# Optimization experiments

Hardware: AMD Instinct MI355X
Metric: run time of the kernel (lower is better)

## Reference

```python
import jax, jax.numpy as jnp
import numpy as np

N_NODES = 50000
N_EDGES = 600000
DIM_H = 128
LN_EPS = 1e-5


def setup_inputs() -> dict:
    key = jax.random.key(0)
    ks = jax.random.split(key, 8)
    s = 1.0 / np.sqrt(DIM_H)
    return {
        "nodes": jax.random.normal(ks[0], (N_NODES, DIM_H), jnp.float32),
        "W_msg": jax.random.normal(ks[1], (DIM_H, DIM_H), jnp.float32) * s,
        "b_msg": jnp.zeros((DIM_H,), jnp.float32),
        "w_ih": jax.random.normal(ks[2], (3 * DIM_H, DIM_H), jnp.float32) * s,
        "w_hh": jax.random.normal(ks[3], (3 * DIM_H, DIM_H), jnp.float32) * s,
        "b_ih": jnp.zeros((3 * DIM_H,), jnp.float32),
        "b_hh": jnp.zeros((3 * DIM_H,), jnp.float32),
        "ln_gamma": jnp.ones((DIM_H,), jnp.float32),
        "ln_beta": jnp.zeros((DIM_H,), jnp.float32),
        "edge_src": jax.random.randint(ks[4], (N_EDGES,), 0, N_NODES, jnp.int32),
        "edge_dst": jax.random.randint(ks[5], (N_EDGES,), 0, N_NODES, jnp.int32),
    }


def _layer_norm(x, gamma, beta):
    mu = jnp.mean(x, axis=-1, keepdims=True)
    var = jnp.mean(jnp.square(x - mu), axis=-1, keepdims=True)
    return gamma * (x - mu) * jax.lax.rsqrt(var + LN_EPS) + beta


def reference(nodes, W_msg, b_msg, w_ih, w_hh, b_ih, b_hh, ln_gamma, ln_beta,
              edge_src, edge_dst):
    n_nodes = nodes.shape[0]
    # send_and_recv: per-edge message from source node, sum-reduce at dest
    msg_e = nodes[edge_src] @ W_msg.T + b_msg            # [E, H] (irregular gather)
    messages = jax.ops.segment_sum(msg_e, edge_dst, num_segments=n_nodes)  # [N, H]
    # global connection: add mean node feature
    msg = messages + jnp.mean(nodes, axis=0)
    # single-step GRU (torch gate layout: r, z, n)
    gi = msg @ w_ih.T + b_ih                             # [N, 3H]
    gh = nodes @ w_hh.T + b_hh                           # [N, 3H]
    i_r, i_z, i_n = jnp.split(gi, 3, axis=-1)
    h_r, h_z, h_n = jnp.split(gh, 3, axis=-1)
    r = jax.nn.sigmoid(i_r + h_r)
    z = jax.nn.sigmoid(i_z + h_z)
    n = jnp.tanh(i_n + r * h_n)
    h_next = (1.0 - z) * n + z * nodes
    # LayerNorm then post-GRU spatial residual with messages
    out = _layer_norm(h_next, ln_gamma, ln_beta)
    out = out + messages
    return out
```

## Files before the change

### kernel.cpp

```cpp
#include <hip/hip_runtime.h>
#include <hip/hip_bf16.h>

#define N_NODES 50000
#define N_EDGES 600000
#define DIM_H   128
#define NPAD    50048
#define NB_SCAN 196

typedef __attribute__((ext_vector_type(8))) short bf16x8;
typedef __attribute__((ext_vector_type(4))) float f32x4;
typedef __attribute__((ext_vector_type(4))) short short4v;

__device__ __forceinline__ short f2bs(float f) {
    __hip_bfloat16 h = __float2bfloat16(f);
    return *reinterpret_cast<short*>(&h);
}
__device__ __forceinline__ float bs2f(short s) {
    unsigned u = ((unsigned)(unsigned short)s) << 16;
    return __builtin_bit_cast(float, u);
}
__device__ __forceinline__ float sigm(float x) { return 1.f / (1.f + __expf(-x)); }
__device__ __forceinline__ float tanh_f(float x) {
    return 2.f / (1.f + __expf(-2.f * x)) - 1.f;
}
__device__ __forceinline__ unsigned pk2(float a, float b) {
    return ((unsigned)(unsigned short)f2bs(b) << 16) | (unsigned)(unsigned short)f2bs(a);
}
__device__ __forceinline__ float unlo(unsigned u) { return bs2f((short)(u & 0xffffu)); }
__device__ __forceinline__ float unhi(unsigned u) { return bs2f((short)(u >> 16)); }

__device__ __forceinline__ void dma16(const void* g, const void* lds_uniform) {
    __builtin_amdgcn_global_load_lds(
        (const __attribute__((address_space(1))) void*)g,
        (__attribute__((address_space(3))) void*)(unsigned)(unsigned long long)lds_uniform,
        16, 0, 0);
}

__global__ __launch_bounds__(256) void prep_k(const float* __restrict__ wmsg,
                                              const float* __restrict__ wih,
                                              const float* __restrict__ whh,
                                              short* __restrict__ wmsgB,
                                              short* __restrict__ wihB,
                                              short* __restrict__ whhB,
                                              int* __restrict__ cnt,
                                              float* __restrict__ colsum,
                                              short* __restrict__ aggTail,
                                              short* __restrict__ nodesTail) {
    int i = blockIdx.x * 256 + threadIdx.x;
    if (i < 16384) wmsgB[i] = f2bs(wmsg[i]);
    if (i < 49152) { wihB[i] = f2bs(wih[i]); whhB[i] = f2bs(whh[i]); }
    if (i < N_NODES) cnt[i] = 0;
    if (i < 128) colsum[i] = 0.f;
    if (i < 1536) {
        short4v z = {0, 0, 0, 0};
        *(short4v*)(aggTail   + i * 4) = z;
        *(short4v*)(nodesTail + i * 4) = z;
    }
}

__global__ __launch_bounds__(256) void colsum_k(const float* __restrict__ nodes,
                                                float* __restrict__ colsum,
                                                short* __restrict__ nodesB) {
    __shared__ float red[8][128];
    const int tid = threadIdx.x;
    const int cg = tid & 31;
    const int rl = tid >> 5;
    float4 acc = {0.f, 0.f, 0.f, 0.f};
    for (int r = blockIdx.x * 8 + rl; r < N_NODES; r += gridDim.x * 8) {
        float4 v = *(const float4*)(nodes + (size_t)r * DIM_H + cg * 4);
        acc.x += v.x; acc.y += v.y; acc.z += v.z; acc.w += v.w;
        *(short4v*)(nodesB + (size_t)r * DIM_H + cg * 4) =
            (short4v){f2bs(v.x), f2bs(v.y), f2bs(v.z), f2bs(v.w)};
    }
    *(float4*)&red[rl][cg * 4] = acc;
    __syncthreads();
    if (tid < 128) {
        float s = 0.f;
#pragma unroll
        for (int i = 0; i < 8; ++i) s += red[i][tid];
        unsafeAtomicAdd(&colsum[tid], s);
    }
}

__global__ __launch_bounds__(256) void hist_k(const int* __restrict__ edst,
                                              int* __restrict__ cnt) {
    int e = (blockIdx.x * 256 + threadIdx.x) * 4;
    if (e + 3 < N_EDGES) {
        int4 d = *(const int4*)(edst + e);
        atomicAdd(&cnt[d.x], 1); atomicAdd(&cnt[d.y], 1);
        atomicAdd(&cnt[d.z], 1); atomicAdd(&cnt[d.w], 1);
    } else {
        for (; e < N_EDGES; ++e) atomicAdd(&cnt[edst[e]], 1);
    }
}

__global__ __launch_bounds__(256) void bsum_k(const int* __restrict__ cnt,
                                              int* __restrict__ bsum) {
    const int t = threadIdx.x;
    int i = blockIdx.x * 256 + t;
    int v = (i < N_NODES) ? cnt[i] : 0;
#pragma unroll
    for (int o = 32; o; o >>= 1) v += __shfl_xor(v, o, 64);
    __shared__ int w4[4];
    if ((t & 63) == 0) w4[t >> 6] = v;
    __syncthreads();
    if (t == 0) bsum[blockIdx.x] = w4[0] + w4[1] + w4[2] + w4[3];
}

__global__ __launch_bounds__(256) void scan2_k(const int* __restrict__ cnt,
                                               const int* __restrict__ bsum,
                                               int* __restrict__ rowptr,
                                               int* __restrict__ pos) {
    const int b = blockIdx.x, t = threadIdx.x;
    const int lane = t & 63, w = t >> 6;
    __shared__ int red[4];
    __shared__ int wsum[4];

    int ov = (t < b) ? bsum[t] : 0;
#pragma unroll
    for (int o = 32; o; o >>= 1) ov += __shfl_xor(ov, o, 64);
    if (lane == 0) red[w] = ov;
    __syncthreads();
    const int offset = red[0] + red[1] + red[2] + red[3];

    int i = b * 256 + t;
    int v = (i < N_NODES) ? cnt[i] : 0;
    int x = v;
#pragma unroll
    for (int o = 1; o < 64; o <<= 1) {
        int y = __shfl_up(x, o, 64);
        if (lane >= o) x += y;
    }
    if (lane == 63) wsum[w] = x;
    __syncthreads();
    int woff = 0;
#pragma unroll
    for (int j = 0; j < 4; ++j)
        if (j < w) woff += wsum[j];
    int excl = offset + woff + (x - v);
    if (i < N_NODES) { rowptr[i] = excl; pos[i] = excl; }
    if (i == N_NODES - 1) rowptr[N_NODES] = excl + v;
}

__global__ __launch_bounds__(256) void reorder_k(const int* __restrict__ esrc,
                                                 const int* __restrict__ edst,
                                                 int* __restrict__ pos,
                                                 int* __restrict__ ssrc) {
    int e = (blockIdx.x * 256 + threadIdx.x) * 4;
    if (e + 3 < N_EDGES) {
        int4 s = *(const int4*)(esrc + e);
        int4 d = *(const int4*)(edst + e);
        ssrc[atomicAdd(&pos[d.x], 1)] = s.x;
        ssrc[atomicAdd(&pos[d.y], 1)] = s.y;
        ssrc[atomicAdd(&pos[d.z], 1)] = s.z;
        ssrc[atomicAdd(&pos[d.w], 1)] = s.w;
    } else {
        for (; e < N_EDGES; ++e) {
            int p = atomicAdd(&pos[edst[e]], 1);
            ssrc[p] = esrc[e];
        }
    }
}

__global__ __launch_bounds__(256) void aggregate_k(const short* __restrict__ nodesB,
                                                   const int* __restrict__ rowptr,
                                                   const int* __restrict__ ssrc,
                                                   short* __restrict__ aggB) {
    const int wid = threadIdx.x >> 6;
    const int lane = threadIdx.x & 63;
    const int g = lane >> 4, l = lane & 15;
    const int n = blockIdx.x * 4 + wid;
    if (n >= N_NODES) return;
    const int s0 = rowptr[n], s1 = rowptr[n + 1];

    float accf[8] = {0.f, 0.f, 0.f, 0.f, 0.f, 0.f, 0.f, 0.f};
    int e = s0 + g;
    for (; e + 4 < s1; e += 8) {
        int sa = ssrc[e], sb = ssrc[e + 4];
        bf16x8 va = *(const bf16x8*)(nodesB + (size_t)sa * DIM_H + l * 8);
        bf16x8 vb = *(const bf16x8*)(nodesB + (size_t)sb * DIM_H + l * 8);
#pragma unroll
        for (int k = 0; k < 8; ++k) accf[k] += bs2f(va[k]) + bs2f(vb[k]);
    }
    if (e < s1) {
        int sa = ssrc[e];
        bf16x8 va = *(const bf16x8*)(nodesB + (size_t)sa * DIM_H + l * 8);
#pragma unroll
        for (int k = 0; k < 8; ++k) accf[k] += bs2f(va[k]);
    }
#pragma unroll
    for (int k = 0; k < 8; ++k) {
        accf[k] += __shfl_xor(accf[k], 32, 64);
        accf[k] += __shfl_xor(accf[k], 16, 64);
    }
    if (g == 0) {
        uint4 ov;
        ov.x = pk2(accf[0], accf[1]);
        ov.y = pk2(accf[2], accf[3]);
        ov.z = pk2(accf[4], accf[5]);
        ov.w = pk2(accf[6], accf[7]);
        *(uint4*)(aggB + (size_t)n * DIM_H + l * 8) = ov;
    }
}

__global__ __launch_bounds__(512) void fused_k(const short* __restrict__ aggB,
                                               const short* __restrict__ nodesB,
                                               const short* __restrict__ wmsgB,
                                               const short* __restrict__ wihB,
                                               const short* __restrict__ whhB,
                                               const float* __restrict__ bmsg,
                                               const float* __restrict__ bih,
                                               const float* __restrict__ bhh,
                                               const int* __restrict__ deg,
                                               const float* __restrict__ colsum,
                                               const float* __restrict__ gamma,
                                               const float* __restrict__ beta,
                                               float* __restrict__ out) {
    __shared__ short Ms[128 * 128];
    __shared__ short Wb[2][64 * 128];
    __shared__ float biasL[1280];

    const int tid = threadIdx.x;
    const int lane = tid & 63, w = tid >> 6;
    const int m0 = blockIdx.x * 128;
    const int r16 = lane & 15, qh = lane >> 4;
    const int wm = w * 16;
    const float invN = 1.0f / N_NODES;

    if (tid < 384) {
        biasL[tid]       = bih[tid];
        biasL[384 + tid] = bhh[tid];
    }
    if (tid < 128) {
        biasL[768  + tid] = bmsg[tid];
        biasL[896  + tid] = colsum[tid] * invN;
        biasL[1024 + tid] = gamma[tid];
        biasL[1152 + tid] = beta[tid];
    }

    bf16x8 aggF[4], nodF[4], msgF[4];
    const size_t rowA = (size_t)(m0 + wm + r16) * 128;
#pragma unroll
    for (int kt = 0; kt < 4; ++kt) {
        aggF[kt] = *(const bf16x8*)(aggB   + rowA + ((kt << 2) + qh) * 8);
        nodF[kt] = *(const bf16x8*)(nodesB + rowA + ((kt << 2) + qh) * 8);
    }
    int4 dgi = *(const int4*)(deg + m0 + wm + qh * 4);

#define STAGE_W(SRC, ROW0, BUF) do {                                         \
    _Pragma("unroll") for (int it = 0; it < 2; ++it) {                       \
        int c = w * 2 + it;                                                  \
        int s = c * 64 + lane;                                               \
        int r = s >> 4, q = s & 15;                                          \
        int g = q ^ (r & 15);                                                \
        dma16((SRC) + (((size_t)((ROW0) + r)) << 7) + (g << 3),              \
              &Wb[BUF][0] + (size_t)c * 512);                                \
    } } while (0)

    STAGE_W(wmsgB, 0, 0);

    f32x4 acc[2][4];
    unsigned rp[2][4][2], inp[2][4][2], np_[2][4][2];

#define CHUNK(BUF, AF, H, RST) do {                                          \
    _Pragma("unroll") for (int kt = 0; kt < 4; ++kt) {                       \
        const int sq = (((kt << 2) + qh) ^ r16) << 3;                        \
        bf16x8 b0 = *(const bf16x8*)&Wb[BUF][(r16     ) * 128 + sq];         \
        bf16x8 b1 = *(const bf16x8*)&Wb[BUF][(r16 + 16) * 128 + sq];         \
        bf16x8 b2 = *(const bf16x8*)&Wb[BUF][(r16 + 32) * 128 + sq];         \
        bf16x8 b3 = *(const bf16x8*)&Wb[BUF][(r16 + 48) * 128 + sq];         \
        f32x4 z4 = {0.f, 0.f, 0.f, 0.f};                                     \
        acc[H][0] = __builtin_amdgcn_mfma_f32_16x16x32_bf16(                 \
            AF[kt], b0, ((RST) && kt == 0) ? z4 : acc[H][0], 0, 0, 0);       \
        acc[H][1] = __builtin_amdgcn_mfma_f32_16x16x32_bf16(                 \
            AF[kt], b1, ((RST) && kt == 0) ? z4 : acc[H][1], 0, 0, 0);       \
        acc[H][2] = __builtin_amdgcn_mfma_f32_16x16x32_bf16(                 \
            AF[kt], b2, ((RST) && kt == 0) ? z4 : acc[H][2], 0, 0, 0);       \
        acc[H][3] = __builtin_amdgcn_mfma_f32_16x16x32_bf16(                 \
            AF[kt], b3, ((RST) && kt == 0) ? z4 : acc[H][3], 0, 0, 0);       \
    } } while (0)

    __syncthreads(); STAGE_W(wmsgB,  64, 1); CHUNK(0, aggF, 0, 1);
    __syncthreads(); STAGE_W(wihB,    0, 0); CHUNK(1, aggF, 1, 1);

    {
        float dgf[4];
        dgf[0] = (m0 + wm + qh * 4 + 0 < N_NODES) ? (float)dgi.x : 0.f;
        dgf[1] = (m0 + wm + qh * 4 + 1 < N_NODES) ? (float)dgi.y : 0.f;
        dgf[2] = (m0 + wm + qh * 4 + 2 < N_NODES) ? (float)dgi.z : 0.f;
        dgf[3] = (m0 + wm + qh * 4 + 3 < N_NODES) ? (float)dgi.w : 0.f;
#pragma unroll
        for (int h = 0; h < 2; ++h)
#pragma unroll
            for (int j = 0; j < 4; ++j) {
                int c = h * 64 + j * 16 + r16;
                float bm = biasL[768 + c], cs = biasL[896 + c];
#pragma unroll
                for (int rr = 0; rr < 4; ++rr) {
                    int lr = wm + qh * 4 + rr;
                    float v = acc[h][j][rr] + dgf[rr] * bm + cs;
                    int slot = (c >> 3) ^ (lr & 15);
                    Ms[lr * 128 + slot * 8 + (c & 7)] = f2bs(v);
                }
            }
#pragma unroll
        for (int kt = 0; kt < 4; ++kt) {
            int kg = (kt << 2) + qh;
            msgF[kt] = *(const bf16x8*)&Ms[(wm + r16) * 128 + ((kg ^ r16) << 3)];
        }
    }

    __syncthreads(); STAGE_W(wihB,   64, 1); CHUNK(0, msgF, 0, 1);
    __syncthreads(); STAGE_W(whhB,    0, 0); CHUNK(1, msgF, 1, 1);
    __syncthreads(); STAGE_W(whhB,   64, 1); CHUNK(0, nodF, 0, 0);
    __syncthreads(); STAGE_W(wihB,  256, 0); CHUNK(1, nodF, 1, 0);
#pragma unroll
    for (int h = 0; h < 2; ++h)
#pragma unroll
        for (int j = 0; j < 4; ++j) {
            int c = h * 64 + j * 16 + r16;
            float b0 = biasL[c] + biasL[384 + c];
            rp[h][j][0] = pk2(sigm(acc[h][j][0] + b0), sigm(acc[h][j][1] + b0));
            rp[h][j][1] = pk2(sigm(acc[h][j][2] + b0), sigm(acc[h][j][3] + b0));
        }

    __syncthreads(); STAGE_W(wihB,  320, 1); CHUNK(0, msgF, 0, 1);
    __syncthreads(); STAGE_W(whhB,  256, 0); CHUNK(1, msgF, 1, 1);
#pragma unroll
    for (int h = 0; h < 2; ++h)
#pragma unroll
        for (int j = 0; j < 4; ++j) {
            int c = h * 64 + j * 16 + r16;
            float bi = biasL[256 + c];
            inp[h][j][0] = pk2(acc[h][j][0] + bi, acc[h][j][1] + bi);
            inp[h][j][1] = pk2(acc[h][j][2] + bi, acc[h][j][3] + bi);
        }

    __syncthreads(); STAGE_W(whhB,  320, 1); CHUNK(0, nodF, 0, 1);
    __syncthreads(); STAGE_W(wihB,  128, 0); CHUNK(1, nodF, 1, 1);
#pragma unroll
    for (int h = 0; h < 2; ++h)
#pragma unroll
        for (int j = 0; j < 4; ++j) {
            int c = h * 64 + j * 16 + r16;
            float bh = biasL[640 + c];
            float n0 = tanh_f(unlo(inp[h][j][0]) + unlo(rp[h][j][0]) * (acc[h][j][0] + bh));
            float n1 = tanh_f(unhi(inp[h][j][0]) + unhi(rp[h][j][0]) * (acc[h][j][1] + bh));
            float n2 = tanh_f(unlo(inp[h][j][1]) + unlo(rp[h][j][1]) * (acc[h][j][2] + bh));
            float n3 = tanh_f(unhi(inp[h][j][1]) + unhi(rp[h][j][1]) * (acc[h][j][3] + bh));
            np_[h][j][0] = pk2(n0, n1);
            np_[h][j][1] = pk2(n2, n3);
        }

    __syncthreads(); STAGE_W(wihB,  192, 1); CHUNK(0, msgF, 0, 1);
    __syncthreads(); STAGE_W(whhB,  128, 0); CHUNK(1, msgF, 1, 1);
    __syncthreads(); STAGE_W(whhB,  192, 1); CHUNK(0, nodF, 0, 0);
    __syncthreads();                         CHUNK(1, nodF, 1, 0);

#pragma unroll
    for (int h = 0; h < 2; ++h)
#pragma unroll
        for (int j = 0; j < 4; ++j) {
            int c = h * 64 + j * 16 + r16;
            float b1 = biasL[128 + c] + biasL[512 + c];
#pragma unroll
            for (int rr = 0; rr < 4; ++rr) {
                int lr = wm + qh * 4 + rr;
                float hv = bs2f(nodesB[(size_t)(m0 + lr) * 128 + c]);
                float z = sigm(acc[h][j][rr] + b1);
                float nv = (rr & 1) ? unhi(np_[h][j][rr >> 1]) : unlo(np_[h][j][rr >> 1]);
                acc[h][j][rr] = (1.f - z) * nv + z * hv;
            }
        }

#pragma unroll
    for (int rr = 0; rr < 4; ++rr) {
        float s = 0.f, q2 = 0.f;
#pragma unroll
        for (int h = 0; h < 2; ++h)
#pragma unroll
            for (int j = 0; j < 4; ++j) {
                float v = acc[h][j][rr];
                s += v; q2 += v * v;
            }
#pragma unroll
        for (int o = 1; o < 16; o <<= 1) {
            s  += __shfl_xor(s, o, 64);
            q2 += __shfl_xor(q2, o, 64);
        }
        int lr = wm + qh * 4 + rr;
        int gm = m0 + lr;
        float mu = s * (1.0f / DIM_H);
        float var = q2 * (1.0f / DIM_H) - mu * mu;
        float rstd = rsqrtf(var + 1e-5f);
        if (gm < N_NODES) {
#pragma unroll
            for (int h = 0; h < 2; ++h)
#pragma unroll
                for (int j = 0; j < 4; ++j) {
                    int c = h * 64 + j * 16 + r16;
                    int slot = (c >> 3) ^ (lr & 15);
                    float resid = bs2f(Ms[lr * 128 + slot * 8 + (c & 7)])
                                - biasL[896 + c];
                    out[(size_t)gm * DIM_H + c] =
                        biasL[1024 + c] * (acc[h][j][rr] - mu) * rstd
                        + biasL[1152 + c] + resid;
                }
        }
    }
#undef CHUNK
#undef STAGE_W
}

extern "C" void kernel_launch(void* const* d_in, const int* in_sizes, int n_in,
                              void* d_out, int out_size, void* d_ws, size_t ws_size,
                              hipStream_t stream) {
    const float* nodes = (const float*)d_in[0];
    const float* Wmsg  = (const float*)d_in[1];
    const float* bmsg  = (const float*)d_in[2];
    const float* wih   = (const float*)d_in[3];
    const float* whh   = (const float*)d_in[4];
    const float* bih   = (const float*)d_in[5];
    const float* bhh   = (const float*)d_in[6];
    const float* gamma = (const float*)d_in[7];
    const float* beta  = (const float*)d_in[8];
    const int* esrc = (const int*)d_in[9];
    const int* edst = (const int*)d_in[10];
    float* out = (float*)d_out;

    char* ws = (char*)d_ws;
    short* aggB   = (short*)ws;
    short* nodesB = (short*)(ws + 12812288);
    short* wmsgB  = (short*)(ws + 25624576);
    short* wihB   = (short*)(ws + 25657344);
    short* whhB   = (short*)(ws + 25755648);
    float* colsum = (float*)(ws + 25853952);
    int*   cnt    = (int*)(ws + 25854464);
    int*   rowptr = (int*)(ws + 26054464);
    int*   pos    = (int*)(ws + 26254480);
    int*   ssrc   = (int*)(ws + 26454480);
    int*   bsum   = (int*)(ws + 28854480);

    short* aggTail   = aggB   + (size_t)N_NODES * DIM_H;
    short* nodesTail = nodesB + (size_t)N_NODES * DIM_H;

    prep_k<<<NB_SCAN, 256, 0, stream>>>(Wmsg, wih, whh, wmsgB, wihB, whhB,
                                        cnt, colsum, aggTail, nodesTail);
    colsum_k<<<512, 256, 0, stream>>>(nodes, colsum, nodesB);

    const int EB4 = (N_EDGES / 4 + 255) / 256;
    hist_k<<<EB4, 256, 0, stream>>>(edst, cnt);
    bsum_k<<<NB_SCAN, 256, 0, stream>>>(cnt, bsum);
    scan2_k<<<NB_SCAN, 256, 0, stream>>>(cnt, bsum, rowptr, pos);
    reorder_k<<<EB4, 256, 0, stream>>>(esrc, edst, pos, ssrc);
    aggregate_k<<<(N_NODES + 3) / 4, 256, 0, stream>>>(nodesB, rowptr, ssrc, aggB);

    const int MB = (N_NODES + 127) / 128;
    fused_k<<<MB, 512, 0, stream>>>(aggB, nodesB, wmsgB, wihB, whhB,
                                    bmsg, bih, bhh, cnt, colsum, gamma, beta, out);
}
```

Before: 238.9 us.

## Merge preprocessing kernels into one cooperative kernel with grid syncs

Replaces six small launches (weight conversion, column sum, histogram, block sums, scan, reorder) with a single cooperative kernel that separates phases using grid-wide syncs. The aim is to remove per-launch overhead and idle gaps between the tiny dependent kernels. In exchange it adds grid.sync costs and ties the grid size to an occupancy query capped at 1024 blocks, which could reduce parallelism in the edge-scatter phases.

```diff
diff --git a/kernel.cpp b/kernel.cpp
--- a/kernel.cpp
+++ b/kernel.cpp
@@ -1,5 +1,8 @@
 #include <hip/hip_runtime.h>
 #include <hip/hip_bf16.h>
+#include <hip/hip_cooperative_groups.h>
+
+namespace cg = cooperative_groups;
 
 #define N_NODES 50000
 #define N_EDGES 600000
@@ -36,128 +39,132 @@
         16, 0, 0);
 }
 
-__global__ __launch_bounds__(256) void prep_k(const float* __restrict__ wmsg,
-                                              const float* __restrict__ wih,
-                                              const float* __restrict__ whh,
-                                              short* __restrict__ wmsgB,
-                                              short* __restrict__ wihB,
-                                              short* __restrict__ whhB,
-                                              int* __restrict__ cnt,
-                                              float* __restrict__ colsum,
-                                              short* __restrict__ aggTail,
-                                              short* __restrict__ nodesTail) {
-    int i = blockIdx.x * 256 + threadIdx.x;
-    if (i < 16384) wmsgB[i] = f2bs(wmsg[i]);
-    if (i < 49152) { wihB[i] = f2bs(wih[i]); whhB[i] = f2bs(whh[i]); }
-    if (i < N_NODES) cnt[i] = 0;
-    if (i < 128) colsum[i] = 0.f;
-    if (i < 1536) {
+__global__ __launch_bounds__(256) void front_k(const float* __restrict__ nodes,
+                                               const float* __restrict__ wmsg,
+                                               const float* __restrict__ wih,
+                                               const float* __restrict__ whh,
+                                               short* __restrict__ wmsgB,
+                                               short* __restrict__ wihB,
+                                               short* __restrict__ whhB,
+                                               int* __restrict__ cnt,
+                                               float* __restrict__ colsum,
+                                               short* __restrict__ aggTail,
+                                               short* __restrict__ nodesTail,
+                                               short* __restrict__ nodesB,
+                                               int* __restrict__ bsum,
+                                               int* __restrict__ rowptr,
+                                               int* __restrict__ pos,
+                                               const int* __restrict__ esrc,
+                                               const int* __restrict__ edst,
+                                               int* __restrict__ ssrc) {
+    cg::grid_group grid = cg::this_grid();
+    const int tid = threadIdx.x;
+    const int gid = blockIdx.x * 256 + tid;
+    const int gsz = gridDim.x * 256;
+
+    for (int i = gid; i < 49152; i += gsz) {
+        wihB[i] = f2bs(wih[i]);
+        whhB[i] = f2bs(whh[i]);
+    }
+    for (int i = gid; i < 16384; i += gsz) wmsgB[i] = f2bs(wmsg[i]);
+    for (int i = gid; i < N_NODES; i += gsz) cnt[i] = 0;
+    if (gid < 128) colsum[gid] = 0.f;
+    for (int i = gid; i < 1536; i += gsz) {
         short4v z = {0, 0, 0, 0};
         *(short4v*)(aggTail   + i * 4) = z;
         *(short4v*)(nodesTail + i * 4) = z;
     }
-}
-
-__global__ __launch_bounds__(256) void colsum_k(const float* __restrict__ nodes,
-                                                float* __restrict__ colsum,
-                                                short* __restrict__ nodesB) {
-    __shared__ float red[8][128];
-    const int tid = threadIdx.x;
-    const int cg = tid & 31;
-    const int rl = tid >> 5;
-    float4 acc = {0.f, 0.f, 0.f, 0.f};
-    for (int r = blockIdx.x * 8 + rl; r < N_NODES; r += gridDim.x * 8) {
-        float4 v = *(const float4*)(nodes + (size_t)r * DIM_H + cg * 4);
-        acc.x += v.x; acc.y += v.y; acc.z += v.z; acc.w += v.w;
-        *(short4v*)(nodesB + (size_t)r * DIM_H + cg * 4) =
-            (short4v){f2bs(v.x), f2bs(v.y), f2bs(v.z), f2bs(v.w)};
-    }
-    *(float4*)&red[rl][cg * 4] = acc;
-    __syncthreads();
-    if (tid < 128) {
-        float s = 0.f;
-#pragma unroll
-        for (int i = 0; i < 8; ++i) s += red[i][tid];
-        unsafeAtomicAdd(&colsum[tid], s);
-    }
-}
-
-__global__ __launch_bounds__(256) void hist_k(const int* __restrict__ edst,
-                                              int* __restrict__ cnt) {
-    int e = (blockIdx.x * 256 + threadIdx.x) * 4;
-    if (e + 3 < N_EDGES) {
-        int4 d = *(const int4*)(edst + e);
-        atomicAdd(&cnt[d.x], 1); atomicAdd(&cnt[d.y], 1);
-        atomicAdd(&cnt[d.z], 1); atomicAdd(&cnt[d.w], 1);
-    } else {
-        for (; e < N_EDGES; ++e) atomicAdd(&cnt[edst[e]], 1);
-    }
-}
-
-__global__ __launch_bounds__(256) void bsum_k(const int* __restrict__ cnt,
-                                              int* __restrict__ bsum) {
-    const int t = threadIdx.x;
-    int i = blockIdx.x * 256 + t;
-    int v = (i < N_NODES) ? cnt[i] : 0;
-#pragma unroll
-    for (int o = 32; o; o >>= 1) v += __shfl_xor(v, o, 64);
-    __shared__ int w4[4];
-    if ((t & 63) == 0) w4[t >> 6] = v;
-    __syncthreads();
-    if (t == 0) bsum[blockIdx.x] = w4[0] + w4[1] + w4[2] + w4[3];
-}
-
-__global__ __launch_bounds__(256) void scan2_k(const int* __restrict__ cnt,
-                                               const int* __restrict__ bsum,
-                                               int* __restrict__ rowptr,
-                                               int* __restrict__ pos) {
-    const int b = blockIdx.x, t = threadIdx.x;
-    const int lane = t & 63, w = t >> 6;
-    __shared__ int red[4];
-    __shared__ int wsum[4];
-
-    int ov = (t < b) ? bsum[t] : 0;
-#pragma unroll
-    for (int o = 32; o; o >>= 1) ov += __shfl_xor(ov, o, 64);
-    if (lane == 0) red[w] = ov;
-    __syncthreads();
-    const int offset = red[0] + red[1] + red[2] + red[3];
-
-    int i = b * 256 + t;
-    int v = (i < N_NODES) ? cnt[i] : 0;
-    int x = v;
-#pragma unroll
-    for (int o = 1; o < 64; o <<= 1) {
-        int y = __shfl_up(x, o, 64);
-        if (lane >= o) x += y;
-    }
-    if (lane == 63) wsum[w] = x;
-    __syncthreads();
-    int woff = 0;
-#pragma unroll
-    for (int j = 0; j < 4; ++j)
-        if (j < w) woff += wsum[j];
-    int excl = offset + woff + (x - v);
-    if (i < N_NODES) { rowptr[i] = excl; pos[i] = excl; }
-    if (i == N_NODES - 1) rowptr[N_NODES] = excl + v;
-}
-
-__global__ __launch_bounds__(256) void reorder_k(const int* __restrict__ esrc,
-                                                 const int* __restrict__ edst,
-                                                 int* __restrict__ pos,
-                                                 int* __restrict__ ssrc) {
-    int e = (blockIdx.x * 256 + threadIdx.x) * 4;
-    if (e + 3 < N_EDGES) {
-        int4 s = *(const int4*)(esrc + e);
-        int4 d = *(const int4*)(edst + e);
-        ssrc[atomicAdd(&pos[d.x], 1)] = s.x;
-        ssrc[atomicAdd(&pos[d.y], 1)] = s.y;
-        ssrc[atomicAdd(&pos[d.z], 1)] = s.z;
-        ssrc[atomicAdd(&pos[d.w], 1)] = s.w;
-    } else {
-        for (; e < N_EDGES; ++e) {
-            int p = atomicAdd(&pos[edst[e]], 1);
-            ssrc[p] = esrc[e];
+    grid.sync();
+
+    for (int e0 = gid * 4; e0 < N_EDGES; e0 += gsz * 4) {
+        if (e0 + 3 < N_EDGES) {
+            int4 d = *(const int4*)(edst + e0);
+            atomicAdd(&cnt[d.x], 1); atomicAdd(&cnt[d.y], 1);
+            atomicAdd(&cnt[d.z], 1); atomicAdd(&cnt[d.w], 1);
+        } else {
+            for (int e = e0; e < N_EDGES; ++e) atomicAdd(&cnt[edst[e]], 1);
+        }
+    }
+    {
+        __shared__ float redB[8][128];
+        const int cgl = tid & 31;
+        const int rl = tid >> 5;
+        float4 a = {0.f, 0.f, 0.f, 0.f};
+        for (int r = blockIdx.x * 8 + rl; r < N_NODES; r += gridDim.x * 8) {
+            float4 v = *(const float4*)(nodes + (size_t)r * DIM_H + cgl * 4);
+            a.x += v.x; a.y += v.y; a.z += v.z; a.w += v.w;
+            *(short4v*)(nodesB + (size_t)r * DIM_H + cgl * 4) =
+                (short4v){f2bs(v.x), f2bs(v.y), f2bs(v.z), f2bs(v.w)};
+        }
+        *(float4*)&redB[rl][cgl * 4] = a;
+        __syncthreads();
+        if (tid < 128) {
+            float s = 0.f;
+#pragma unroll
+            for (int i = 0; i < 8; ++i) s += redB[i][tid];
+            unsafeAtomicAdd(&colsum[tid], s);
+        }
+    }
+    grid.sync();
+
+    if (blockIdx.x < NB_SCAN) {
+        __shared__ int w4[4];
+        int i = blockIdx.x * 256 + tid;
+        int v = (i < N_NODES) ? cnt[i] : 0;
+#pragma unroll
+        for (int o = 32; o; o >>= 1) v += __shfl_xor(v, o, 64);
+        if ((tid & 63) == 0) w4[tid >> 6] = v;
+        __syncthreads();
+        if (tid == 0) bsum[blockIdx.x] = w4[0] + w4[1] + w4[2] + w4[3];
+    }
+    grid.sync();
+
+    if (blockIdx.x < NB_SCAN) {
+        const int b = blockIdx.x;
+        const int lane = tid & 63, w = tid >> 6;
+        __shared__ int redS[4];
+        __shared__ int wsum[4];
+
+        int ov = (tid < b) ? bsum[tid] : 0;
+#pragma unroll
+        for (int o = 32; o; o >>= 1) ov += __shfl_xor(ov, o, 64);
+        if (lane == 0) redS[w] = ov;
+        __syncthreads();
+        const int offset = redS[0] + redS[1] + redS[2] + redS[3];
+
+        int i = b * 256 + tid;
+        int v = (i < N_NODES) ? cnt[i] : 0;
+        int x = v;
+#pragma unroll
+        for (int o = 1; o < 64; o <<= 1) {
+            int y = __shfl_up(x, o, 64);
+            if (lane >= o) x += y;
+        }
+        if (lane == 63) wsum[w] = x;
+        __syncthreads();
+        int woff = 0;
+#pragma unroll
+        for (int j = 0; j < 4; ++j)
+            if (j < w) woff += wsum[j];
+        int excl = offset + woff + (x - v);
+        if (i < N_NODES) { rowptr[i] = excl; pos[i] = excl; }
+        if (i == N_NODES - 1) rowptr[N_NODES] = excl + v;
+    }
+    grid.sync();
+
+    for (int e0 = gid * 4; e0 < N_EDGES; e0 += gsz * 4) {
+        if (e0 + 3 < N_EDGES) {
+            int4 s = *(const int4*)(esrc + e0);
+            int4 d = *(const int4*)(edst + e0);
+            ssrc[atomicAdd(&pos[d.x], 1)] = s.x;
+            ssrc[atomicAdd(&pos[d.y], 1)] = s.y;
+            ssrc[atomicAdd(&pos[d.z], 1)] = s.z;
+            ssrc[atomicAdd(&pos[d.w], 1)] = s.w;
+        } else {
+            for (int e = e0; e < N_EDGES; ++e) {
+                int p = atomicAdd(&pos[edst[e]], 1);
+                ssrc[p] = esrc[e];
+            }
         }
     }
 }
@@ -444,15 +451,27 @@
     short* aggTail   = aggB   + (size_t)N_NODES * DIM_H;
     short* nodesTail = nodesB + (size_t)N_NODES * DIM_H;
 
-    prep_k<<<NB_SCAN, 256, 0, stream>>>(Wmsg, wih, whh, wmsgB, wihB, whhB,
-                                        cnt, colsum, aggTail, nodesTail);
-    colsum_k<<<512, 256, 0, stream>>>(nodes, colsum, nodesB);
-
-    const int EB4 = (N_EDGES / 4 + 255) / 256;
-    hist_k<<<EB4, 256, 0, stream>>>(edst, cnt);
-    bsum_k<<<NB_SCAN, 256, 0, stream>>>(cnt, bsum);
-    scan2_k<<<NB_SCAN, 256, 0, stream>>>(cnt, bsum, rowptr, pos);
-    reorder_k<<<EB4, 256, 0, stream>>>(esrc, edst, pos, ssrc);
+    static int s_grid = 0;
+    if (s_grid == 0) {
+        int perCU = 0;
+        hipError_t err = hipOccupancyMaxActiveBlocksPerMultiprocessor(
+            &perCU, front_k, 256, 0);
+        if (err != hipSuccess || perCU < 1) perCU = 1;
+        long cap = (long)perCU * 256;
+        s_grid = (int)(cap < 1024 ? cap : 1024);
+        if (s_grid < NB_SCAN) s_grid = NB_SCAN;
+    }
+
+    void* fargs[] = {
+        (void*)&nodes, (void*)&Wmsg, (void*)&wih, (void*)&whh,
+        (void*)&wmsgB, (void*)&wihB, (void*)&whhB,
+        (void*)&cnt, (void*)&colsum, (void*)&aggTail, (void*)&nodesTail,
+        (void*)&nodesB, (void*)&bsum, (void*)&rowptr, (void*)&pos,
+        (void*)&esrc, (void*)&edst, (void*)&ssrc
+    };
+    hipLaunchCooperativeKernel((const void*)front_k, dim3(s_grid), dim3(256),
+                               fargs, 0, stream);
+
     aggregate_k<<<(N_NODES + 3) / 4, 256, 0, stream>>>(nodesB, rowptr, ssrc, aggB);
 
     const int MB = (N_NODES + 127) / 128;
```

Measured after the change: 633.4 us. +165.1%, slower.
